# Kernel tuning notes

Hardware: AMD Instinct MI355X
Metric: run time of the kernel (lower is better)

## Reference

```python
import jax, jax.numpy as jnp
import numpy as np
import math

B, LL, LP = 16, 256, 1024
HID, H = 128, 8
SCALE = math.sqrt(HID)


def setup_inputs() -> dict:
    key = jax.random.key(0)
    ks = jax.random.split(key, 20)
    s = 0.02
    inp = {
        "ligand": jax.random.normal(ks[0], (B, LL, HID), jnp.float32),
        "prot": jax.random.normal(ks[1], (B, LP, HID), jnp.float32),
        "inter": jax.random.uniform(ks[2], (B, 1, LL, LP), jnp.float32),
        # projection weights stored as [in, out] (x @ W + b)
        "Wl1": jax.random.normal(ks[3], (HID, HID * H), jnp.float32) * s,
        "bl1": jnp.zeros((HID * H,), jnp.float32),
        "Wl2": jax.random.normal(ks[4], (HID, HID * H), jnp.float32) * s,
        "bl2": jnp.zeros((HID * H,), jnp.float32),
        "Wp1": jax.random.normal(ks[5], (HID, HID * H), jnp.float32) * s,
        "bp1": jnp.zeros((HID * H,), jnp.float32),
        "Wp2": jax.random.normal(ks[6], (HID, HID * H), jnp.float32) * s,
        "bp2": jnp.zeros((HID * H,), jnp.float32),
        "W11": jax.random.normal(ks[7], (HID * H, HID), jnp.float32) * s,
        "b11": jnp.zeros((HID,), jnp.float32),
        "W12": jax.random.normal(ks[8], (2 * HID, HID), jnp.float32) * s,
        "b12": jnp.zeros((HID,), jnp.float32),
        "W21": jax.random.normal(ks[9], (HID * H, HID), jnp.float32) * s,
        "b21": jnp.zeros((HID,), jnp.float32),
        "W22": jax.random.normal(ks[10], (2 * HID, HID), jnp.float32) * s,
        "b22": jnp.zeros((HID,), jnp.float32),
    }
    return inp


def _heads(x):
    # [B, L, H*D] -> [B, H, L, D]
    b, l, _ = x.shape
    return x.reshape(b, l, H, HID).transpose(0, 2, 1, 3)


def reference(ligand, prot, inter, Wl1, bl1, Wl2, bl2, Wp1, bp1, Wp2, bp2,
              W11, b11, W12, b12, W21, b21, W22, b22):
    relu = jax.nn.relu
    l1 = _heads(relu(ligand @ Wl1 + bl1))   # [B,H,LL,D]
    l2 = _heads(relu(ligand @ Wl2 + bl2))   # [B,H,LL,D]
    p1 = _heads(relu(prot @ Wp1 + bp1))     # [B,H,LP,D]
    p2 = _heads(relu(prot @ Wp2 + bp2))     # [B,H,LP,D]

    energy = jnp.einsum('bhld,bhpd->bhlp', l1, p1) / SCALE
    att = jax.nn.softmax(energy * inter, axis=-1)  # dropout is identity at eval

    # ligand branch: att @ prot2 -> [B,LL,H*D]
    lig3 = jnp.einsum('bhlp,bhpd->blhd', att, p2).reshape(B, LL, H * HID)
    lig3 = jnp.concatenate([lig3 @ W11 + b11, ligand], axis=2)
    lig3 = relu(lig3 @ W12 + b12)

    # protein branch: att^T @ ligand2 -> [B,LP,H*D]
    prot3 = jnp.einsum('bhlp,bhld->bphd', att, l2).reshape(B, LP, H * HID)
    prot3 = jnp.concatenate([prot3 @ W21 + b21, prot], axis=2)
    prot3 = relu(prot3 @ W22 + b22)
    return (lig3, prot3)
```

## Files before the change

### kernel.cpp

```cpp
#include <hip/hip_runtime.h>
#include <hip/hip_bf16.h>

typedef unsigned short u16;
typedef __attribute__((ext_vector_type(4))) float f32x4;
typedef __attribute__((ext_vector_type(4))) unsigned int u32x4;
typedef __attribute__((ext_vector_type(4))) unsigned short u16x4;
typedef __attribute__((ext_vector_type(8))) __bf16 bf16x8;

__device__ inline float u2f(u16 u) {
    union { unsigned int i; float f; } x; x.i = ((unsigned int)u) << 16; return x.f;
}
__device__ inline u16 f2u(float f) {
    __hip_bfloat16 b = __float2bfloat16(f);
    return *reinterpret_cast<u16*>(&b);
}
__device__ inline f32x4 mfma16(bf16x8 a, bf16x8 b, f32x4 c) {
    return __builtin_amdgcn_mfma_f32_16x16x32_bf16(a, b, c, 0, 0, 0);
}
__device__ inline void gload_lds16(const u16* g, u16* l) {
    __builtin_amdgcn_global_load_lds(
        (const __attribute__((address_space(1))) unsigned int*)g,
        (__attribute__((address_space(3))) unsigned int*)l, 16, 0, 0);
}

__global__ __launch_bounds__(256)
void proj_kernel(const u16* __restrict__ ligb, const u16* __restrict__ protb,
                 const u16* __restrict__ Wl1t, const u16* __restrict__ Wl2t,
                 const u16* __restrict__ Wp1t, const u16* __restrict__ Wp2t,
                 const float* __restrict__ bl1, const float* __restrict__ bl2,
                 const float* __restrict__ bp1, const float* __restrict__ bp2,
                 u16* __restrict__ l1v, u16* __restrict__ l2tv,
                 u16* __restrict__ p1v, u16* __restrict__ p2tv)
{
    __shared__ __align__(16) u16 As[128 * 64];
    __shared__ __align__(16) u16 Bs[128 * 64];
    const int y = blockIdx.y;
    const u16* A; const u16* B; const float* bias; u16* Out;
    int mode, logL, my;
    if (y < 32)       { A = ligb;  B = Wl1t; bias = bl1; Out = l1v;  mode = 1; logL = 8;  my = y; }
    else if (y < 64)  { A = ligb;  B = Wl2t; bias = bl2; Out = l2tv; mode = 3; logL = 8;  my = y - 32; }
    else if (y < 192) { A = protb; B = Wp1t; bias = bp1; Out = p1v;  mode = 1; logL = 10; my = y - 64; }
    else              { A = protb; B = Wp2t; bias = bp2; Out = p2tv; mode = 3; logL = 10; my = y - 192; }
    const int n0 = blockIdx.x * 128, m0 = my * 128;
    const int tid = threadIdx.x;
    const int w = tid >> 6, lane = tid & 63, q = lane >> 4, li = lane & 15;
    const int wr = w >> 1, wc = w & 1;

    const int srow = tid >> 3;
    const int cg = (tid & 7) ^ (srow & 7);
    const int ldsbase = ((tid >> 6) * 8) * 64;

    f32x4 acc[4][4];
    #pragma unroll
    for (int i = 0; i < 4; i++)
        #pragma unroll
        for (int j = 0; j < 4; j++) acc[i][j] = (f32x4){0.f, 0.f, 0.f, 0.f};

    #pragma unroll
    for (int kt = 0; kt < 128; kt += 64) {
        const u16* Ab = A + (long)m0 * 128 + kt + cg * 8;
        const u16* Bb = B + (long)n0 * 128 + kt + cg * 8;
        #pragma unroll
        for (int c = 0; c < 4; c++) {
            gload_lds16(Ab + (long)(c * 32 + srow) * 128, &As[ldsbase + c * 32 * 64]);
            gload_lds16(Bb + (long)(c * 32 + srow) * 128, &Bs[ldsbase + c * 32 * 64]);
        }
        __syncthreads();
        #pragma unroll
        for (int s = 0; s < 2; s++) {
            const int cp = ((s * 4 + q) ^ (li & 7)) * 8;
            bf16x8 av[4], bv[4];
            #pragma unroll
            for (int i = 0; i < 4; i++)
                av[i] = *(bf16x8*)&As[(wr * 64 + i * 16 + li) * 64 + cp];
            #pragma unroll
            for (int j = 0; j < 4; j++)
                bv[j] = *(bf16x8*)&Bs[(wc * 64 + j * 16 + li) * 64 + cp];
            #pragma unroll
            for (int i = 0; i < 4; i++)
                #pragma unroll
                for (int j = 0; j < 4; j++)
                    acc[i][j] = mfma16(av[i], bv[j], acc[i][j]);
        }
        __syncthreads();
    }

    const int Lm = (1 << logL) - 1;
    #pragma unroll
    for (int i = 0; i < 4; i++) {
        #pragma unroll
        for (int j = 0; j < 4; j++) {
            const int col = n0 + wc * 64 + j * 16 + li;
            const float bvs = bias[col];
            if (mode == 3) {
                const int row0 = m0 + wr * 64 + i * 16 + q * 4;
                long base = ((long)(((row0 >> logL) * 8 + (col >> 7)) * 128
                            + (col & 127)) << logL) + (row0 & Lm);
                u16x4 o;
                #pragma unroll
                for (int r = 0; r < 4; r++)
                    o[r] = f2u(fmaxf(acc[i][j][r] + bvs, 0.f));
                *(u16x4*)(Out + base) = o;
            } else {
                #pragma unroll
                for (int r = 0; r < 4; r++) {
                    const int row = m0 + wr * 64 + i * 16 + q * 4 + r;
                    long addr = ((long)((row >> logL) * 8 + (col >> 7)) << (logL + 7))
                              + ((long)(row & Lm) << 7) + (col & 127);
                    Out[addr] = f2u(fmaxf(acc[i][j][r] + bvs, 0.f));
                }
            }
        }
    }
}

__global__ __launch_bounds__(512)
void av_kernel(const u16* __restrict__ att, const u16* __restrict__ p2t,
               const u16* __restrict__ l2t,
               u16* __restrict__ lig3, u16* __restrict__ prot3)
{
    __shared__ __align__(16) u16 As[256 * 64];
    __shared__ __align__(16) u16 Bs[128 * 64];
    __shared__ __align__(16) u16 T[64 * 256];
    const int bid = blockIdx.x;
    const int tid = threadIdx.x;
    const int w = tid >> 6, lane = tid & 63, q = lane >> 4, li = lane & 15;
    const int wr = w >> 1, wc = w & 1;

    f32x4 acc[4][4];
    #pragma unroll
    for (int i = 0; i < 4; i++)
        #pragma unroll
        for (int j = 0; j < 4; j++) acc[i][j] = (f32x4){0.f, 0.f, 0.f, 0.f};

    if (bid < 128) {
        const int bh = bid;
        const u16* A = att + (long)bh * 262144;
        const u16* B = p2t + (long)bh * 131072;
        const int srow = tid >> 3;
        const int cg = (tid & 7) ^ (srow & 7);
        const int ldsbase = ((tid >> 6) * 8) * 64;

        for (int kt = 0; kt < 1024; kt += 64) {
            const u16* Ab = A + kt + cg * 8;
            const u16* Bb = B + kt + cg * 8;
            #pragma unroll
            for (int c = 0; c < 4; c++)
                gload_lds16(Ab + (long)(c * 64 + srow) * 1024,
                            &As[ldsbase + c * 64 * 64]);
            #pragma unroll
            for (int c = 0; c < 2; c++)
                gload_lds16(Bb + (long)(c * 64 + srow) * 1024,
                            &Bs[ldsbase + c * 64 * 64]);
            __syncthreads();
            #pragma unroll
            for (int s = 0; s < 2; s++) {
                const int cp = ((s * 4 + q) ^ (li & 7)) * 8;
                bf16x8 av[4], bv[4];
                #pragma unroll
                for (int i = 0; i < 4; i++)
                    av[i] = *(bf16x8*)&As[(wr * 64 + i * 16 + li) * 64 + cp];
                #pragma unroll
                for (int j = 0; j < 4; j++)
                    bv[j] = *(bf16x8*)&Bs[(wc * 64 + j * 16 + li) * 64 + cp];
                #pragma unroll
                for (int i = 0; i < 4; i++)
                    #pragma unroll
                    for (int j = 0; j < 4; j++)
                        acc[i][j] = mfma16(av[i], bv[j], acc[i][j]);
            }
            __syncthreads();
        }

        const long obase = ((long)(bh >> 3) * 256) * 1024 + (long)(bh & 7) * 128;
        #pragma unroll
        for (int i = 0; i < 4; i++)
            #pragma unroll
            for (int j = 0; j < 4; j++) {
                const int col = wc * 64 + j * 16 + li;
                #pragma unroll
                for (int r = 0; r < 4; r++) {
                    const int row = wr * 64 + i * 16 + q * 4 + r;
                    lig3[obase + (long)row * 1024 + col] = f2u(acc[i][j][r]);
                }
            }
    } else {
        const int pb = bid - 128;
        const int bh = pb >> 2;
        const int m0 = (pb & 3) * 256;
        const u16* A = att + (long)bh * 262144;
        const u16* B = l2t + (long)bh * 32768;
        const int w6 = tid >> 6;
        const int i5 = (tid >> 5) & 1;
        const int srow = tid >> 3;
        const int cg = (tid & 7) ^ (srow & 7);
        const int bldsbase = w6 * 8 * 64;

        for (int kt = 0; kt < 256; kt += 64) {
            #pragma unroll
            for (int c = 0; c < 4; c++) {
                gload_lds16(A + (long)(kt + w6 * 8 + c * 2 + i5) * 1024
                              + m0 + (tid & 31) * 8,
                            &T[w6 * 2048 + c * 512]);
            }
            #pragma unroll
            for (int c = 0; c < 2; c++)
                gload_lds16(B + (long)(c * 64 + srow) * 256 + kt + cg * 8,
                            &Bs[bldsbase + c * 64 * 64]);
            __syncthreads();

            #pragma unroll
            for (int pass = 0; pass < 4; pass++) {
                const int p = pass * 64 + (tid & 63);
                union { u16 e[8]; u32x4 v; } tmp;
                #pragma unroll
                for (int e = 0; e < 8; e++)
                    tmp.e[e] = T[(w6 * 8 + e) * 256 + p];
                *(u32x4*)&As[p * 64 + ((w6 ^ (p & 7)) * 8)] = tmp.v;
            }
            __syncthreads();

            #pragma unroll
            for (int s = 0; s < 2; s++) {
                const int cp = ((s * 4 + q) ^ (li & 7)) * 8;
                bf16x8 av[4], bv[4];
                #pragma unroll
                for (int i = 0; i < 4; i++)
                    av[i] = *(bf16x8*)&As[(wr * 64 + i * 16 + li) * 64 + cp];
                #pragma unroll
                for (int j = 0; j < 4; j++)
                    bv[j] = *(bf16x8*)&Bs[(wc * 64 + j * 16 + li) * 64 + cp];
                #pragma unroll
                for (int i = 0; i < 4; i++)
                    #pragma unroll
                    for (int j = 0; j < 4; j++)
                        acc[i][j] = mfma16(av[i], bv[j], acc[i][j]);
            }
            __syncthreads();
        }

        const long obase = ((long)(bh >> 3) * 1024 + m0) * 1024 + (long)(bh & 7) * 128;
        #pragma unroll
        for (int i = 0; i < 4; i++)
            #pragma unroll
            for (int j = 0; j < 4; j++) {
                const int col = wc * 64 + j * 16 + li;
                #pragma unroll
                for (int r = 0; r < 4; r++) {
                    const int row = wr * 64 + i * 16 + q * 4 + r;
                    prot3[obase + (long)row * 1024 + col] = f2u(acc[i][j][r]);
                }
            }
    }
}

__global__ __launch_bounds__(256)
void finals_kernel(const u16* __restrict__ lig3, const u16* __restrict__ ligb,
                   const u16* __restrict__ WstL, const float* __restrict__ bcL,
                   float* __restrict__ out0,
                   const u16* __restrict__ prot3, const u16* __restrict__ protb,
                   const u16* __restrict__ WstP, const float* __restrict__ bcP,
                   float* __restrict__ out1)
{
    __shared__ __align__(16) u16 As[128 * 64];
    __shared__ __align__(16) u16 Bs[128 * 64];
    const int y = blockIdx.y;
    const u16 *A, *A2, *B; const float* bias; float* Out; int my;
    if (y < 32) { A = lig3;  A2 = ligb;  B = WstL; bias = bcL; Out = out0; my = y; }
    else        { A = prot3; A2 = protb; B = WstP; bias = bcP; Out = out1; my = y - 32; }
    const int m0 = my * 128;
    const int tid = threadIdx.x;
    const int w = tid >> 6, lane = tid & 63, q = lane >> 4, li = lane & 15;
    const int wr = w >> 1, wc = w & 1;

    const int srow = tid >> 3;
    const int cg = (tid & 7) ^ (srow & 7);
    const int ldsbase = ((tid >> 6) * 8) * 64;

    f32x4 acc[4][4];
    #pragma unroll
    for (int i = 0; i < 4; i++)
        #pragma unroll
        for (int j = 0; j < 4; j++) acc[i][j] = (f32x4){0.f, 0.f, 0.f, 0.f};

    for (int kt = 0; kt < 1152; kt += 64) {
        const u16* Abase; long lda; int ktA;
        if (kt >= 1024) { Abase = A2; lda = 128; ktA = kt - 1024; }
        else            { Abase = A;  lda = 1024; ktA = kt; }
        const u16* Ab = Abase + (long)m0 * lda + ktA + cg * 8;
        const u16* Bb = B + kt + cg * 8;
        #pragma unroll
        for (int c = 0; c < 4; c++) {
            gload_lds16(Ab + (long)(c * 32 + srow) * lda,  &As[ldsbase + c * 32 * 64]);
            gload_lds16(Bb + (long)(c * 32 + srow) * 1152, &Bs[ldsbase + c * 32 * 64]);
        }
        __syncthreads();
        #pragma unroll
        for (int s = 0; s < 2; s++) {
            const int cp = ((s * 4 + q) ^ (li & 7)) * 8;
            bf16x8 av[4], bv[4];
            #pragma unroll
            for (int i = 0; i < 4; i++)
                av[i] = *(bf16x8*)&As[(wr * 64 + i * 16 + li) * 64 + cp];
            #pragma unroll
            for (int j = 0; j < 4; j++)
                bv[j] = *(bf16x8*)&Bs[(wc * 64 + j * 16 + li) * 64 + cp];
            #pragma unroll
            for (int i = 0; i < 4; i++)
                #pragma unroll
                for (int j = 0; j < 4; j++)
                    acc[i][j] = mfma16(av[i], bv[j], acc[i][j]);
        }
        __syncthreads();
    }

    #pragma unroll
    for (int i = 0; i < 4; i++)
        #pragma unroll
        for (int j = 0; j < 4; j++) {
            const int col = wc * 64 + j * 16 + li;
            const float bvs = bias[col];
            #pragma unroll
            for (int r = 0; r < 4; r++) {
                const int row = m0 + wr * 64 + i * 16 + q * 4 + r;
                Out[(long)row * 128 + col] = fmaxf(acc[i][j][r] + bvs, 0.f);
            }
        }
}

__global__ __launch_bounds__(256)
void attn_kernel(const u16* __restrict__ l1, const u16* __restrict__ p1,
                 const float* __restrict__ inter, u16* __restrict__ att)
{
    __shared__ __align__(16) u16 As[16][136];
    __shared__ float wmax[4][16];
    __shared__ float wsum[4][16];
    const int bh = blockIdx.y;
    const int b  = bh >> 3;
    const int m0 = blockIdx.x * 16;
    const int tid = threadIdx.x;
    const int w = tid >> 6, lane = tid & 63, q = lane >> 4, li = lane & 15;

    {
        const int row = tid >> 4, col = (tid & 15) * 8;
        *(u32x4*)&As[row][col] =
            *(const u32x4*)(l1 + ((long)bh * 256 + m0 + row) * 128 + col);
    }
    __syncthreads();

    bf16x8 af[4];
    #pragma unroll
    for (int s = 0; s < 4; s++) af[s] = *(bf16x8*)&As[li][s * 32 + q * 8];

    float sv[16][4];
    const float rscale = 0.08838834764831845f;
    for (int t = 0; t < 16; t++) {
        const int n0 = w * 256 + t * 16;
        const u16* bp = p1 + ((long)bh * 1024 + n0 + li) * 128 + q * 8;
        f32x4 acc = (f32x4){0.f, 0.f, 0.f, 0.f};
        #pragma unroll
        for (int s = 0; s < 4; s++) {
            bf16x8 bfg = *(const bf16x8*)(bp + s * 32);
            acc = mfma16(af[s], bfg, acc);
        }
        const int pcol = n0 + li;
        #pragma unroll
        for (int r = 0; r < 4; r++) {
            const int l = m0 + q * 4 + r;
            float iv = inter[((long)b * 256 + l) * 1024 + pcol];
            sv[t][r] = acc[r] * rscale * iv;
        }
    }

    float rmax[4];
    #pragma unroll
    for (int r = 0; r < 4; r++) {
        float m = sv[0][r];
        #pragma unroll
        for (int t = 1; t < 16; t++) m = fmaxf(m, sv[t][r]);
        for (int d = 1; d < 16; d <<= 1) m = fmaxf(m, __shfl_xor(m, d, 64));
        rmax[r] = m;
    }
    if (li == 0) {
        #pragma unroll
        for (int r = 0; r < 4; r++) wmax[w][q * 4 + r] = rmax[r];
    }
    __syncthreads();
    float gmax[4];
    #pragma unroll
    for (int r = 0; r < 4; r++) {
        gmax[r] = fmaxf(fmaxf(wmax[0][q * 4 + r], wmax[1][q * 4 + r]),
                        fmaxf(wmax[2][q * 4 + r], wmax[3][q * 4 + r]));
    }
    #pragma unroll
    for (int r = 0; r < 4; r++) {
        float s = 0.f;
        #pragma unroll
        for (int t = 0; t < 16; t++) {
            float e = __expf(sv[t][r] - gmax[r]);
            sv[t][r] = e;
            s += e;
        }
        for (int d = 1; d < 16; d <<= 1) s += __shfl_xor(s, d, 64);
        if (li == 0) wsum[w][q * 4 + r] = s;
    }
    __syncthreads();
    float inv[4];
    #pragma unroll
    for (int r = 0; r < 4; r++) {
        float s = wsum[0][q * 4 + r] + wsum[1][q * 4 + r]
                + wsum[2][q * 4 + r] + wsum[3][q * 4 + r];
        inv[r] = 1.f / s;
    }
    for (int t = 0; t < 16; t++) {
        #pragma unroll
        for (int r = 0; r < 4; r++) {
            const int l = m0 + q * 4 + r;
            const int pcol = w * 256 + t * 16 + li;
            att[((long)bh * 256 + l) * 1024 + pcol] = f2u(sv[t][r] * inv[r]);
        }
    }
}

struct TPF { const float* src; u16* dst; int R; int C; };
struct TPF8 { TPF t[8]; };

__global__ __launch_bounds__(256)
void cvtw_kernel(TPF8 args)
{
    TPF tp = args.t[blockIdx.z];
    const int c0 = blockIdx.x * 32, r0 = blockIdx.y * 32;
    if (c0 >= tp.C || r0 >= tp.R) return;
    __shared__ u16 tile[32][33];
    const int tx = threadIdx.x & 31, ty = threadIdx.x >> 5;
    #pragma unroll
    for (int i = 0; i < 4; i++)
        tile[ty + i * 8][tx] = f2u(tp.src[(long)(r0 + ty + i * 8) * tp.C + c0 + tx]);
    __syncthreads();
    #pragma unroll
    for (int i = 0; i < 4; i++)
        tp.dst[(long)(c0 + ty + i * 8) * tp.R + r0 + tx] = tile[tx][ty + i * 8];
}

__global__ __launch_bounds__(256)
void wcomb_kernel(const u16* __restrict__ Wm0, const u16* __restrict__ Wo0,
                  const float* __restrict__ bm0, const float* __restrict__ bo0,
                  u16* __restrict__ Wst0, float* __restrict__ bc0,
                  const u16* __restrict__ Wm1, const u16* __restrict__ Wo1,
                  const float* __restrict__ bm1, const float* __restrict__ bo1,
                  u16* __restrict__ Wst1, float* __restrict__ bc1)
{
    const int zz = blockIdx.y;
    const u16* Wm = zz ? Wm1 : Wm0;
    const u16* Wo = zz ? Wo1 : Wo0;
    const float* bmid = zz ? bm1 : bm0;
    const float* bout = zz ? bo1 : bo0;
    u16* Wst = zz ? Wst1 : Wst0;
    float* bc = zz ? bc1 : bc0;
    const int n = blockIdx.x;
    const int tid = threadIdx.x;
    __shared__ float wrow[128];
    if (tid < 128) wrow[tid] = u2f(Wo[n * 256 + tid]);
    __syncthreads();
    for (int k = tid; k < 1024; k += 256) {
        float acc = 0.f;
        #pragma unroll 4
        for (int j = 0; j < 128; j++) acc += wrow[j] * u2f(Wm[(long)j * 1024 + k]);
        Wst[(long)n * 1152 + k] = f2u(acc);
    }
    if (tid < 128) Wst[(long)n * 1152 + 1024 + tid] = Wo[n * 256 + 128 + tid];
    if (tid == 0) {
        float acc = bout[n];
        for (int j = 0; j < 128; j++) acc += bmid[j] * wrow[j];
        bc[n] = acc;
    }
}

__global__ __launch_bounds__(256)
void cvt2_kernel(const float* __restrict__ a, u16* __restrict__ da, int na,
                 const float* __restrict__ b, u16* __restrict__ db, int nb)
{
    const int zz = blockIdx.y;
    const float* s = zz ? b : a;
    u16* d = zz ? db : da;
    const int n = zz ? nb : na;
    const int i = (blockIdx.x * 256 + threadIdx.x) * 4;
    if (i >= n) return;
    const float4 v = *(const float4*)(s + i);
    u16x4 o;
    o.x = f2u(v.x); o.y = f2u(v.y); o.z = f2u(v.z); o.w = f2u(v.w);
    *(u16x4*)(d + i) = o;
}

extern "C" void kernel_launch(void* const* d_in, const int* in_sizes, int n_in,
                              void* d_out, int out_size, void* d_ws, size_t ws_size,
                              hipStream_t stream)
{
    (void)in_sizes; (void)n_in; (void)out_size; (void)ws_size;
    const float* ligand = (const float*)d_in[0];
    const float* prot   = (const float*)d_in[1];
    const float* inter  = (const float*)d_in[2];
    const float* Wl1 = (const float*)d_in[3];  const float* bl1 = (const float*)d_in[4];
    const float* Wl2 = (const float*)d_in[5];  const float* bl2 = (const float*)d_in[6];
    const float* Wp1 = (const float*)d_in[7];  const float* bp1 = (const float*)d_in[8];
    const float* Wp2 = (const float*)d_in[9];  const float* bp2 = (const float*)d_in[10];
    const float* W11 = (const float*)d_in[11]; const float* b11 = (const float*)d_in[12];
    const float* W12 = (const float*)d_in[13]; const float* b12 = (const float*)d_in[14];
    const float* W21 = (const float*)d_in[15]; const float* b21 = (const float*)d_in[16];
    const float* W22 = (const float*)d_in[17]; const float* b22 = (const float*)d_in[18];

    float* out0 = (float*)d_out;
    float* out1 = out0 + (size_t)16 * 256 * 128;

    u16* ws = (u16*)d_ws;
    size_t off = 0;
    auto alloc = [&](size_t n) { u16* p = ws + off; off += n; return p; };
    u16* ligb  = alloc(524288);
    u16* protb = alloc(2097152);
    u16* l1v   = alloc(4194304);
    u16* l2t   = alloc(4194304);
    u16* p1v   = alloc(16777216);
    u16* p2t   = alloc(16777216);
    u16* attv  = alloc(33554432);
    u16* lig3  = alloc(4194304);
    u16* prot3 = alloc(16777216);
    u16* Wl1t  = alloc(131072);
    u16* Wl2t  = alloc(131072);
    u16* Wp1t  = alloc(131072);
    u16* Wp2t  = alloc(131072);
    u16* W11t  = alloc(131072);
    u16* W21t  = alloc(131072);
    u16* W12t  = alloc(32768);
    u16* W22t  = alloc(32768);
    u16* WstL  = alloc(147456);
    u16* WstP  = alloc(147456);
    float* bcL = (float*)alloc(256);
    float* bcP = (float*)alloc(256);

    cvt2_kernel<<<dim3(2048, 2), 256, 0, stream>>>(
        ligand, ligb, 524288, prot, protb, 2097152);

    TPF8 tp;
    tp.t[0] = {Wl1, Wl1t, 128, 1024};
    tp.t[1] = {Wl2, Wl2t, 128, 1024};
    tp.t[2] = {Wp1, Wp1t, 128, 1024};
    tp.t[3] = {Wp2, Wp2t, 128, 1024};
    tp.t[4] = {W11, W11t, 1024, 128};
    tp.t[5] = {W21, W21t, 1024, 128};
    tp.t[6] = {W12, W12t, 256, 128};
    tp.t[7] = {W22, W22t, 256, 128};
    cvtw_kernel<<<dim3(32, 32, 8), 256, 0, stream>>>(tp);

    wcomb_kernel<<<dim3(128, 2), 256, 0, stream>>>(
        W11t, W12t, b11, b12, WstL, bcL,
        W21t, W22t, b21, b22, WstP, bcP);

    proj_kernel<<<dim3(8, 320), 256, 0, stream>>>(
        ligb, protb, Wl1t, Wl2t, Wp1t, Wp2t,
        bl1, bl2, bp1, bp2, l1v, l2t, p1v, p2t);

    attn_kernel<<<dim3(16, 128), 256, 0, stream>>>(l1v, p1v, inter, attv);

    av_kernel<<<dim3(640), 512, 0, stream>>>(attv, p2t, l2t, lig3, prot3);

    finals_kernel<<<dim3(1, 160), 256, 0, stream>>>(
        lig3, ligb, WstL, bcL, out0,
        prot3, protb, WstP, bcP, out1);
}
```

Measured before the change: 329.2 us.

## Stage attention scores in LDS and pre-convert inter mask to bf16

```diff
diff --git a/kernel.cpp b/kernel.cpp
--- a/kernel.cpp
+++ b/kernel.cpp
@@ -5,6 +5,7 @@
 typedef __attribute__((ext_vector_type(4))) float f32x4;
 typedef __attribute__((ext_vector_type(4))) unsigned int u32x4;
 typedef __attribute__((ext_vector_type(4))) unsigned short u16x4;
+typedef __attribute__((ext_vector_type(8))) unsigned short u16x8;
 typedef __attribute__((ext_vector_type(8))) __bf16 bf16x8;
 
 __device__ inline float u2f(u16 u) {
@@ -328,97 +329,88 @@
         }
 }
 
-__global__ __launch_bounds__(256)
+__global__ __launch_bounds__(256, 5)
 void attn_kernel(const u16* __restrict__ l1, const u16* __restrict__ p1,
-                 const float* __restrict__ inter, u16* __restrict__ att)
-{
-    __shared__ __align__(16) u16 As[16][136];
-    __shared__ float wmax[4][16];
-    __shared__ float wsum[4][16];
+                 const u16* __restrict__ interb, u16* __restrict__ att)
+{
+    __shared__ __align__(16) u16 S[16 * 1024];
     const int bh = blockIdx.y;
     const int b  = bh >> 3;
     const int m0 = blockIdx.x * 16;
     const int tid = threadIdx.x;
-    const int w = tid >> 6, lane = tid & 63, q = lane >> 4, li = lane & 15;
+    const float rscale = 0.08838834764831845f;
 
     {
-        const int row = tid >> 4, col = (tid & 15) * 8;
-        *(u32x4*)&As[row][col] =
-            *(const u32x4*)(l1 + ((long)bh * 256 + m0 + row) * 128 + col);
+        const int w = tid >> 6, lane = tid & 63, q = lane >> 4, li = lane & 15;
+        bf16x8 af[4];
+        const u16* lp = l1 + ((long)bh * 256 + m0 + li) * 128 + q * 8;
+        #pragma unroll
+        for (int s = 0; s < 4; s++) af[s] = *(const bf16x8*)(lp + s * 32);
+        const int sw = q << 4;
+        #pragma unroll 4
+        for (int t = 0; t < 16; t++) {
+            const int n0 = w * 256 + t * 16;
+            const u16* bp = p1 + ((long)bh * 1024 + n0 + li) * 128 + q * 8;
+            f32x4 acc = (f32x4){0.f, 0.f, 0.f, 0.f};
+            #pragma unroll
+            for (int s = 0; s < 4; s++)
+                acc = mfma16(af[s], *(const bf16x8*)(bp + s * 32), acc);
+            #pragma unroll
+            for (int r = 0; r < 4; r++) {
+                const int row = q * 4 + r;
+                S[(row << 10) + ((n0 + li) ^ sw)] = f2u(acc[r] * rscale);
+            }
+        }
     }
     __syncthreads();
 
-    bf16x8 af[4];
-    #pragma unroll
-    for (int s = 0; s < 4; s++) af[s] = *(bf16x8*)&As[li][s * 32 + q * 8];
-
-    float sv[16][4];
-    const float rscale = 0.08838834764831845f;
-    for (int t = 0; t < 16; t++) {
-        const int n0 = w * 256 + t * 16;
-        const u16* bp = p1 + ((long)bh * 1024 + n0 + li) * 128 + q * 8;
-        f32x4 acc = (f32x4){0.f, 0.f, 0.f, 0.f};
-        #pragma unroll
-        for (int s = 0; s < 4; s++) {
-            bf16x8 bfg = *(const bf16x8*)(bp + s * 32);
-            acc = mfma16(af[s], bfg, acc);
-        }
-        const int pcol = n0 + li;
-        #pragma unroll
-        for (int r = 0; r < 4; r++) {
-            const int l = m0 + q * 4 + r;
-            float iv = inter[((long)b * 256 + l) * 1024 + pcol];
-            sv[t][r] = acc[r] * rscale * iv;
-        }
-    }
-
-    float rmax[4];
-    #pragma unroll
-    for (int r = 0; r < 4; r++) {
-        float m = sv[0][r];
-        #pragma unroll
-        for (int t = 1; t < 16; t++) m = fmaxf(m, sv[t][r]);
-        for (int d = 1; d < 16; d <<= 1) m = fmaxf(m, __shfl_xor(m, d, 64));
-        rmax[r] = m;
-    }
-    if (li == 0) {
-        #pragma unroll
-        for (int r = 0; r < 4; r++) wmax[w][q * 4 + r] = rmax[r];
-    }
-    __syncthreads();
-    float gmax[4];
-    #pragma unroll
-    for (int r = 0; r < 4; r++) {
-        gmax[r] = fmaxf(fmaxf(wmax[0][q * 4 + r], wmax[1][q * 4 + r]),
-                        fmaxf(wmax[2][q * 4 + r], wmax[3][q * 4 + r]));
-    }
-    #pragma unroll
-    for (int r = 0; r < 4; r++) {
-        float s = 0.f;
-        #pragma unroll
-        for (int t = 0; t < 16; t++) {
-            float e = __expf(sv[t][r] - gmax[r]);
-            sv[t][r] = e;
-            s += e;
-        }
-        for (int d = 1; d < 16; d <<= 1) s += __shfl_xor(s, d, 64);
-        if (li == 0) wsum[w][q * 4 + r] = s;
-    }
-    __syncthreads();
-    float inv[4];
-    #pragma unroll
-    for (int r = 0; r < 4; r++) {
-        float s = wsum[0][q * 4 + r] + wsum[1][q * 4 + r]
-                + wsum[2][q * 4 + r] + wsum[3][q * 4 + r];
-        inv[r] = 1.f / s;
-    }
-    for (int t = 0; t < 16; t++) {
-        #pragma unroll
-        for (int r = 0; r < 4; r++) {
-            const int l = m0 + q * 4 + r;
-            const int pcol = w * 256 + t * 16 + li;
-            att[((long)bh * 256 + l) * 1024 + pcol] = f2u(sv[t][r] * inv[r]);
-        }
+    const int row = tid >> 4;
+    const int lj  = tid & 15;
+    const int l   = m0 + row;
+    const int sw2 = (row >> 2) << 4;
+    const u16* ib = interb + ((long)b * 256 + l) * 1024;
+
+    float mx = -1e30f;
+    #pragma unroll
+    for (int blk = 0; blk < 8; blk++) {
+        const int c = blk * 128 + lj * 8;
+        u16* sp = &S[(row << 10) + (c ^ sw2)];
+        u16x8 s8 = *(u16x8*)sp;
+        u16x8 i8 = *(const u16x8*)(ib + c);
+        u16x8 o8;
+        #pragma unroll
+        for (int e = 0; e < 8; e++) {
+            float v = u2f(s8[e]) * u2f(i8[e]);
+            mx = fmaxf(mx, v);
+            o8[e] = f2u(v);
+        }
+        *(u16x8*)sp = o8;
+    }
+    #pragma unroll
+    for (int d = 1; d < 16; d <<= 1) mx = fmaxf(mx, __shfl_xor(mx, d, 64));
+
+    float z = 0.f;
+    #pragma unroll
+    for (int blk = 0; blk < 8; blk++) {
+        const int c = blk * 128 + lj * 8;
+        u16x8 p8 = *(u16x8*)&S[(row << 10) + (c ^ sw2)];
+        #pragma unroll
+        for (int e = 0; e < 8; e++) z += __expf(u2f(p8[e]) - mx);
+    }
+    #pragma unroll
+    for (int d = 1; d < 16; d <<= 1) z += __shfl_xor(z, d, 64);
+    const float inv = 1.f / z;
+
+    u16* op = att + ((long)bh * 256 + l) * 1024;
+    #pragma unroll
+    for (int blk = 0; blk < 8; blk++) {
+        const int c = blk * 128 + lj * 8;
+        u16x8 p8 = *(u16x8*)&S[(row << 10) + (c ^ sw2)];
+        u16x8 o8;
+        #pragma unroll
+        for (int e = 0; e < 8; e++)
+            o8[e] = f2u(__expf(u2f(p8[e]) - mx) * inv);
+        *(u16x8*)(op + c) = o8;
     }
 }
 
@@ -477,13 +469,14 @@
 }
 
 __global__ __launch_bounds__(256)
-void cvt2_kernel(const float* __restrict__ a, u16* __restrict__ da, int na,
-                 const float* __restrict__ b, u16* __restrict__ db, int nb)
+void cvt3_kernel(const float* __restrict__ a, u16* __restrict__ da, int na,
+                 const float* __restrict__ b, u16* __restrict__ db, int nb,
+                 const float* __restrict__ c, u16* __restrict__ dc, int nc)
 {
     const int zz = blockIdx.y;
-    const float* s = zz ? b : a;
-    u16* d = zz ? db : da;
-    const int n = zz ? nb : na;
+    const float* s = zz == 0 ? a : (zz == 1 ? b : c);
+    u16* d = zz == 0 ? da : (zz == 1 ? db : dc);
+    const int n = zz == 0 ? na : (zz == 1 ? nb : nc);
     const int i = (blockIdx.x * 256 + threadIdx.x) * 4;
     if (i >= n) return;
     const float4 v = *(const float4*)(s + i);
@@ -537,8 +530,10 @@
     float* bcL = (float*)alloc(256);
     float* bcP = (float*)alloc(256);
 
-    cvt2_kernel<<<dim3(2048, 2), 256, 0, stream>>>(
-        ligand, ligb, 524288, prot, protb, 2097152);
+    u16* interb = lig3;
+
+    cvt3_kernel<<<dim3(4096, 3), 256, 0, stream>>>(
+        ligand, ligb, 524288, prot, protb, 2097152, inter, interb, 4194304);
 
     TPF8 tp;
     tp.t[0] = {Wl1, Wl1t, 128, 1024};
@@ -559,7 +554,7 @@
         ligb, protb, Wl1t, Wl2t, Wp1t, Wp2t,
         bl1, bl2, bp1, bp2, l1v, l2t, p1v, p2t);
 
-    attn_kernel<<<dim3(16, 128), 256, 0, stream>>>(l1v, p1v, inter, attv);
+    attn_kernel<<<dim3(16, 128), 256, 0, stream>>>(l1v, p1v, interb, attv);
 
     av_kernel<<<dim3(640), 512, 0, stream>>>(attv, p2t, l2t, lig3, prot3);
 
```

New measurement: 320.1 us. 2.8% less time.
